# Optimization experiments

Measured on AMD Instinct MI355X. Metric: run time of the kernel, lower is better.

## Reference

```python
import jax, jax.numpy as jnp
import numpy as np

B, C, H, W, HEADS = 8, 96, 128, 128, 6  # dim=96, num_heads=6


def _conv(x, w, b=None, groups=1, pad=0):
    # NCHW conv, OIHW weights; groups for depthwise convs
    y = jax.lax.conv_general_dilated(
        x, w, window_strides=(1, 1), padding=[(pad, pad), (pad, pad)],
        dimension_numbers=('NCHW', 'OIHW', 'NCHW'), feature_group_count=groups)
    return y if b is None else y + b[None, :, None, None]


def setup_inputs() -> dict:
    key = jax.random.key(0)
    ks = jax.random.split(key, 12)
    s = lambda k, shape, fan: jax.random.normal(k, shape, jnp.float32) * (1.0 / np.sqrt(fan))
    return {
        "x": jax.random.normal(ks[0], (B, C, H, W), jnp.float32),
        "y": jax.random.normal(ks[1], (B, C, H, W), jnp.float32),
        "w_pos":   s(ks[2], (2 * C, 2 * C, 1, 1), 2 * C),      # pos 1x1, no bias
        "w_qv":    s(ks[3], (2 * C, C, 1, 1), C),              # qv_ 1x1
        "w_qv_dw": s(ks[4], (2 * C, 1, 3, 3), 9),              # qv depthwise 3x3
        "w_kv":    s(ks[5], (2 * C, C, 1, 1), C),              # kv 1x1
        "w_kv_dw": s(ks[6], (2 * C, 1, 3, 3), 9),              # kv depthwise 3x3
        "w_proj":  s(ks[7], (2 * C, C, 1, 1), C),              # project_out 1x1
        "w_fuse":  s(ks[8], (C, 2 * C, 3, 3), 2 * C * 9),      # v_fuse 3x3 (bias=True)
        "b_fuse":  jnp.zeros((C,), jnp.float32),
        "temperature": jnp.ones((HEADS, 1, 1), jnp.float32),
    }


def reference(x, y, w_pos, w_qv, w_qv_dw, w_kv, w_kv_dw, w_proj, w_fuse, b_fuse, temperature):
    b, c, h, w = x.shape
    xy_pos = _conv(jnp.concatenate([x, y], axis=1), w_pos)
    qv_ = _conv(_conv(x, w_qv), w_qv_dw, groups=2 * c, pad=1)
    kv = _conv(_conv(y, w_kv), w_kv_dw, groups=2 * c, pad=1)
    q, v_ = jnp.split(qv_, 2, axis=1)
    k, v0 = jnp.split(kv, 2, axis=1)
    v = _conv(jnp.concatenate([v0, v_], axis=1), w_fuse, b_fuse, pad=1)
    ch = c // HEADS
    resh = lambda t: t.reshape(b, HEADS, ch, h * w)  # b head c (h w)
    qh, kh, vh = resh(q), resh(k), resh(v)
    # F.normalize(dim=-1): L2 over spatial positions, eps=1e-12
    nrm = lambda t: t / jnp.maximum(jnp.linalg.norm(t, axis=-1, keepdims=True), 1e-12)
    qh, kh = nrm(qh), nrm(kh)
    attn = jax.nn.softmax(jnp.einsum('bhcn,bhdn->bhcd', qh, kh) * temperature, axis=-1)
    out = jnp.einsum('bhcd,bhdn->bhcn', attn, vh).reshape(b, c, h, w)
    return _conv(out, w_proj) + xy_pos
```

## Files before the change

### kernel.cpp

```cpp
#include <hip/hip_runtime.h>
#include <math.h>

#define NB 8
#define NSP 16384
#define NHEADS 6
#define BT ((long)NB * NSP)

typedef __attribute__((ext_vector_type(8))) short bf8_t;
typedef __attribute__((ext_vector_type(4))) float f4_t;
typedef unsigned short u16;

#define MFMA(A,B,C) __builtin_amdgcn_mfma_f32_16x16x32_bf16((A),(B),(C),0,0,0)

__device__ __forceinline__ u16 f2b(float f) {
  union { float f; unsigned u; } v; v.f = f;
  unsigned r = v.u + 0x7FFFu + ((v.u >> 16) & 1u);
  return (u16)(r >> 16);
}
__device__ __forceinline__ float b2f(u16 h) {
  union { unsigned u; float f; } v; v.u = ((unsigned)h) << 16; return v.f;
}


__global__ __launch_bounds__(256)
void pack_w_k(const float* __restrict__ wqv, const float* __restrict__ wkv,
              const float* __restrict__ wpos, const float* __restrict__ wfuse,
              u16* __restrict__ wqv_b, u16* __restrict__ wkv_b,
              u16* __restrict__ wpos_b, u16* __restrict__ wfA) {
  int i = blockIdx.x * 256 + threadIdx.x;
  if (i < 18432) { wqv_b[i] = f2b(wqv[i]); wkv_b[i] = f2b(wkv[i]); }
  if (i < 36864) wpos_b[i] = f2b(wpos[i]);
  if (i < 165888) {
    int kl = i & 31; int rest = i >> 5;
    int oc = rest % 96, kc = rest / 96;
    int c6 = kc / 9, tap = kc % 9;
    int icf = c6 * 32 + kl;
    wfA[i] = f2b(wfuse[(oc * 192 + icf) * 9 + tap]);
  }
}

__global__ __launch_bounds__(256)
void tcast_k(const float* __restrict__ x, const float* __restrict__ y,
             u16* __restrict__ xb, u16* __restrict__ yb) {
  const float* src = blockIdx.y ? y : x;
  u16* dst = blockIdx.y ? yb : xb;
  int t = threadIdx.x;
  long n  = (long)blockIdx.x * 64 + (t & 63);
  long b  = n >> 14; long ni = n & 16383;
  int c8b = t >> 6;
  for (int i = 0; i < 3; ++i) {
    int c8 = c8b + i * 4;
    bf8_t pk;
#pragma unroll
    for (int j = 0; j < 8; ++j)
      pk[j] = (short)f2b(src[(b * 96 + c8 * 8 + j) * NSP + ni]);
    *(bf8_t*)(dst + ((long)c8 * BT + n) * 8) = pk;
  }
}

__global__ __launch_bounds__(256)
void conv1x1_k(const u16* __restrict__ Bx, const u16* __restrict__ A,
               u16* __restrict__ out) {
  int t = threadIdx.x, w = t >> 6, lane = t & 63;
  int q = lane >> 4, l15 = lane & 15;
  long n0 = (long)blockIdx.x * 64;
  f4_t acc[3][4] = {};
#pragma unroll
  for (int kc = 0; kc < 3; ++kc) {
    bf8_t af[3], bfr[4];
#pragma unroll
    for (int mf = 0; mf < 3; ++mf)
      af[mf] = *(const bf8_t*)(A + (w * 48 + mf * 16 + l15) * 96 + kc * 32 + q * 8);
#pragma unroll
    for (int nf = 0; nf < 4; ++nf)
      bfr[nf] = *(const bf8_t*)(Bx + ((long)(kc * 4 + q) * BT + n0 + nf * 16 + l15) * 8);
#pragma unroll
    for (int mf = 0; mf < 3; ++mf)
#pragma unroll
      for (int nf = 0; nf < 4; ++nf)
        acc[mf][nf] = MFMA(af[mf], bfr[nf], acc[mf][nf]);
  }
#pragma unroll
  for (int mf = 0; mf < 3; ++mf)
#pragma unroll
    for (int nf = 0; nf < 4; ++nf) {
      union { u16 us[4]; uint2 v; } pk;
#pragma unroll
      for (int r = 0; r < 4; ++r) pk.us[r] = f2b(acc[mf][nf][r]);
      long n = n0 + nf * 16 + l15;
      int g = w * 6 + mf * 2 + (q >> 1);
      *(uint2*)(out + ((long)g * BT + n) * 8 + (q & 1) * 4) = pk.v;
    }
}

__global__ __launch_bounds__(256)
void dw_k(const u16* __restrict__ qv0, const u16* __restrict__ kv0,
          const float* __restrict__ wqvd, const float* __restrict__ wkvd,
          u16* __restrict__ qL, u16* __restrict__ kL, u16* __restrict__ fin) {
  int t = threadIdx.x;
  int sel = blockIdx.y;
  int bx = blockIdx.x;
  int gq = bx % 6;
  int rowid = bx / 6;
  long b = rowid >> 7; int r = rowid & 127;
  int wv = __builtin_amdgcn_readfirstlane(t >> 6);
  int g = gq * 4 + wv;
  int l = t & 63;
  int c0 = l * 2;

  const u16* src  = sel ? kv0 : qv0;
  const float* wd = sel ? wkvd : wqvd;

  float wgt[8][9];
#pragma unroll
  for (int cc = 0; cc < 8; ++cc)
#pragma unroll
    for (int tp = 0; tp < 9; ++tp)
      wgt[cc][tp] = wd[g * 72 + cc * 9 + tp];

  const u16* sg = src + (long)g * BT * 8;
  float acc[2][8] = {};
#pragma unroll
  for (int dy = -1; dy <= 1; ++dy) {
    int rr = r + dy;
    if ((unsigned)rr >= 128u) continue;
    long nb = (b << 14) + ((long)rr << 7);
    float xq[4][8];
#pragma unroll
    for (int j = 0; j < 4; ++j) {
      int col = c0 - 1 + j;
      uint4 cv = make_uint4(0u, 0u, 0u, 0u);
      if ((unsigned)col < 128u)
        cv = *(const uint4*)(sg + (nb + col) * 8);
      const unsigned* cu = (const unsigned*)&cv;
#pragma unroll
      for (int k = 0; k < 4; ++k) {
        union { unsigned u; float f; } lo, hi;
        lo.u = cu[k] << 16; hi.u = cu[k] & 0xFFFF0000u;
        xq[j][2 * k] = lo.f; xq[j][2 * k + 1] = hi.f;
      }
    }
#pragma unroll
    for (int dx = 0; dx < 3; ++dx) {
      int tp = (dy + 1) * 3 + dx;
#pragma unroll
      for (int px = 0; px < 2; ++px)
#pragma unroll
        for (int cc = 0; cc < 8; ++cc)
          acc[px][cc] += wgt[cc][tp] * xq[px + dx][cc];
    }
  }
  u16* dst; long gi;
  if (g < 12) { dst = sel ? kL : qL; gi = g; }
  else        { dst = fin; gi = sel ? (g - 12) : g; }
  u16* dp = dst + (gi * BT + (b << 14) + ((long)r << 7) + c0) * 8;
#pragma unroll
  for (int px = 0; px < 2; ++px) {
    union { u16 us[8]; uint4 v; } pk;
#pragma unroll
    for (int cc = 0; cc < 8; ++cc) pk.us[cc] = f2b(acc[px][cc]);
    *(uint4*)(dp + px * 8) = pk.v;
  }
}

__global__ __launch_bounds__(512)
void fuse_k(const u16* __restrict__ fin, const u16* __restrict__ wfA,
            const float* __restrict__ bfuse, u16* __restrict__ vout) {
  __shared__ __align__(16) u16 AL[2][192 * 36];
  int t = threadIdx.x, w = t >> 6, lane = t & 63;
  int q = lane >> 4, l15 = lane & 15;
  int bid = (int)blockIdx.x;
  bid = (bid & 7) * 64 + (bid >> 3);
  long n0 = (long)bid * 256;
  long b = n0 >> 14; int nimg0 = (int)(n0 & 16383);

  f4_t acc[6][2];
#pragma unroll
  for (int mf = 0; mf < 6; ++mf) {
#pragma unroll
    for (int rg = 0; rg < 4; ++rg) {
      float bv = bfuse[mf * 16 + q * 4 + rg];
      acc[mf][0][rg] = bv; acc[mf][1][rg] = bv;
    }
  }
  int ni_[2], r_[2], pw_[2];
#pragma unroll
  for (int nf = 0; nf < 2; ++nf) {
    ni_[nf] = nimg0 + w * 32 + nf * 16 + l15;
    r_[nf] = ni_[nf] >> 7; pw_[nf] = ni_[nf] & 127;
  }
  for (int i = t; i < 768; i += 512)
    *(f4_t*)(&AL[0][(i >> 2) * 36 + (i & 3) * 8]) = *(const f4_t*)(wfA + i * 8);
  __syncthreads();

  for (int kc2 = 0; kc2 < 27; ++kc2) {
    int cur = kc2 & 1;
    if (kc2 < 26) {
      const u16* srcw = wfA + (kc2 + 1) * 6144;
      for (int i = t; i < 768; i += 512)
        *(f4_t*)(&AL[cur ^ 1][(i >> 2) * 36 + (i & 3) * 8]) = *(const f4_t*)(srcw + i * 8);
    }
#pragma unroll
    for (int h = 0; h < 2; ++h) {
      int kc = kc2 * 2 + h;
      int c6 = kc / 9, tap = kc % 9;
      int dy = tap / 3 - 1, dx = tap % 3 - 1;
      const u16* src = fin + (long)(c6 * 4 + q) * BT * 8;
      bf8_t bfr[2];
#pragma unroll
      for (int nf = 0; nf < 2; ++nf) {
        bf8_t v = {0,0,0,0,0,0,0,0};
        int rr = r_[nf] + dy, cc = pw_[nf] + dx;
        if ((unsigned)rr < 128u && (unsigned)cc < 128u)
          v = *(const bf8_t*)(src + ((b << 14) + (long)ni_[nf] + dy * 128 + dx) * 8);
        bfr[nf] = v;
      }
      bf8_t af[6];
#pragma unroll
      for (int mf = 0; mf < 6; ++mf)
        af[mf] = *(const bf8_t*)(&AL[cur][(h * 96 + mf * 16 + l15) * 36 + q * 8]);
#pragma unroll
      for (int mf = 0; mf < 6; ++mf) {
        acc[mf][0] = MFMA(af[mf], bfr[0], acc[mf][0]);
        acc[mf][1] = MFMA(af[mf], bfr[1], acc[mf][1]);
      }
    }
    __syncthreads();
  }
#pragma unroll
  for (int mf = 0; mf < 6; ++mf)
#pragma unroll
    for (int nf = 0; nf < 2; ++nf) {
      union { u16 us[4]; uint2 v; } pk;
#pragma unroll
      for (int rg = 0; rg < 4; ++rg) pk.us[rg] = f2b(acc[mf][nf][rg]);
      long n = n0 + w * 32 + nf * 16 + l15;
      int gg = mf * 2 + (q >> 1);
      *(uint2*)(vout + ((long)gg * BT + n) * 8 + (q & 1) * 4) = pk.v;
    }
}

__global__ __launch_bounds__(256)
void ssq_k(const u16* __restrict__ qL, const u16* __restrict__ kL,
           float* __restrict__ ssq) {
  int c8 = blockIdx.x;
  int b = blockIdx.y >> 1, z = blockIdx.y & 1;
  const u16* src = (z ? kL : qL) + ((long)c8 * BT + (b << 14)) * 8;
  float ss[8] = {};
  int n0 = blockIdx.z * 4096, nend = n0 + 4096;
  for (int n = n0 + threadIdx.x; n < nend; n += 256) {
    bf8_t v = *(const bf8_t*)(src + (long)n * 8);
#pragma unroll
    for (int j = 0; j < 8; ++j) { float f = b2f((u16)v[j]); ss[j] += f * f; }
  }
#pragma unroll
  for (int off = 32; off; off >>= 1)
#pragma unroll
    for (int j = 0; j < 8; ++j) ss[j] += __shfl_down(ss[j], off);
  __shared__ float red[4][8];
  int lane = threadIdx.x & 63, wv = threadIdx.x >> 6;
  if (!lane)
#pragma unroll
    for (int j = 0; j < 8; ++j) red[wv][j] = ss[j];
  __syncthreads();
  if (threadIdx.x < 8) {
    int j = threadIdx.x;
    float tot = red[0][j] + red[1][j] + red[2][j] + red[3][j];
    atomicAdd(&ssq[(z * NB + b) * 96 + c8 * 8 + j], tot);
  }
}

__global__ __launch_bounds__(256)
void qk_k(const u16* __restrict__ qL, const u16* __restrict__ kL,
          float* __restrict__ logits) {
  int s = blockIdx.x, h = blockIdx.y, b = blockIdx.z;
  int t = threadIdx.x, c = t >> 4, d = t & 15;
  __shared__ u16 Qs[64 * 16], Ks[64 * 16];
  float acc = 0.f;
  int p = t >> 2, c4 = (t & 3) * 4;
  int ch2 = 2 * h + (c4 >> 3), e = c4 & 7;
  long cb = (long)ch2 * BT + (b << 14) + s * 512;
  for (int it = 0; it < 8; ++it) {
    __syncthreads();
    long a = (cb + it * 64 + p) * 8 + e;
    *(uint2*)(&Qs[p * 16 + c4]) = *(const uint2*)(qL + a);
    *(uint2*)(&Ks[p * 16 + c4]) = *(const uint2*)(kL + a);
    __syncthreads();
#pragma unroll 8
    for (int pp = 0; pp < 64; ++pp)
      acc += b2f(Qs[pp * 16 + c]) * b2f(Ks[pp * 16 + d]);
  }
  atomicAdd(&logits[((b * NHEADS + h) * 16 + c) * 16 + d], acc);
}

__global__ __launch_bounds__(256)
void softmax_k(const float* __restrict__ logits, const float* __restrict__ ssq,
               const float* __restrict__ temp, float* __restrict__ attn) {
  int t0 = blockIdx.x * 256 + threadIdx.x;
  if (t0 >= NB * 96) return;
  int b = t0 / 96, c96 = t0 % 96;
  int h = c96 >> 4, c = c96 & 15;
  float iq = 1.f / fmaxf(sqrtf(ssq[b * 96 + c96]), 1e-12f);
  float tp = temp[h];
  const float* lp = logits + ((b * NHEADS + h) * 16 + c) * 16;
  const float* sk = ssq + NB * 96 + b * 96 + h * 16;
  float s[16], mx = -3.4e38f;
#pragma unroll
  for (int d = 0; d < 16; ++d) {
    float ik = 1.f / fmaxf(sqrtf(sk[d]), 1e-12f);
    float l = lp[d] * iq * ik * tp;
    s[d] = l; mx = fmaxf(mx, l);
  }
  float sum = 0.f;
#pragma unroll
  for (int d = 0; d < 16; ++d) { s[d] = __expf(s[d] - mx); sum += s[d]; }
  float rr = 1.f / sum;
  float* ap = attn + ((b * NHEADS + h) * 16 + c) * 16;
#pragma unroll
  for (int d = 0; d < 16; ++d) ap[d] = s[d] * rr;
}

__global__ __launch_bounds__(256)
void wattn_k(const float* __restrict__ wproj, const float* __restrict__ attn,
             u16* __restrict__ Wp) {
  int b = blockIdx.x, t = threadIdx.x;
  __shared__ float at[1536];
  for (int i = t; i < 1536; i += 256) at[i] = attn[b * 1536 + i];
  __syncthreads();
  for (int i = t; i < 192 * 96; i += 256) {
    int oc = i / 96, e = i % 96;
    int h = e >> 4, d = e & 15;
    float s = 0.f;
#pragma unroll
    for (int c = 0; c < 16; ++c)
      s += wproj[oc * 96 + h * 16 + c] * at[(h * 16 + c) * 16 + d];
    Wp[(long)b * 18432 + i] = f2b(s);
  }
}

__global__ __launch_bounds__(256)
void final_k(const u16* __restrict__ Wp, const u16* __restrict__ wpos_b,
             const u16* __restrict__ v, const u16* __restrict__ xb,
             const u16* __restrict__ yb, float* __restrict__ out) {
  int t = threadIdx.x, w = t >> 6, lane = t & 63;
  int q = lane >> 4, l15 = lane & 15;
  long n0 = (long)blockIdx.x * 64;
  long b = n0 >> 14; int ni0 = (int)(n0 & 16383);
  f4_t acc[3][4] = {};
  const u16* Ab0 = Wp + b * 18432;
#pragma unroll
  for (int kc = 0; kc < 9; ++kc) {
    const u16 *Asrc, *Bsrc; int astr, koff, gB;
    if (kc < 3)      { Asrc = Ab0;    astr = 96;  koff = kc * 32;            Bsrc = v;  gB = kc * 4 + q; }
    else if (kc < 6) { Asrc = wpos_b; astr = 192; koff = (kc - 3) * 32;      Bsrc = xb; gB = (kc - 3) * 4 + q; }
    else             { Asrc = wpos_b; astr = 192; koff = 96 + (kc - 6) * 32; Bsrc = yb; gB = (kc - 6) * 4 + q; }
    bf8_t af[3], bfr[4];
#pragma unroll
    for (int mf = 0; mf < 3; ++mf)
      af[mf] = *(const bf8_t*)(Asrc + (w * 48 + mf * 16 + l15) * astr + koff + q * 8);
#pragma unroll
    for (int nf = 0; nf < 4; ++nf)
      bfr[nf] = *(const bf8_t*)(Bsrc + ((long)gB * BT + n0 + nf * 16 + l15) * 8);
#pragma unroll
    for (int mf = 0; mf < 3; ++mf)
#pragma unroll
      for (int nf = 0; nf < 4; ++nf)
        acc[mf][nf] = MFMA(af[mf], bfr[nf], acc[mf][nf]);
  }
#pragma unroll
  for (int mf = 0; mf < 3; ++mf)
#pragma unroll
    for (int nf = 0; nf < 4; ++nf)
#pragma unroll
      for (int rg = 0; rg < 4; ++rg) {
        int oc = w * 48 + mf * 16 + q * 4 + rg;
        out[(b * 192 + oc) * (long)NSP + ni0 + nf * 16 + l15] = acc[mf][nf][rg];
      }
}

extern "C" void kernel_launch(void* const* d_in, const int* in_sizes, int n_in,
                              void* d_out, int out_size, void* d_ws, size_t ws_size,
                              hipStream_t stream) {
  const float* x     = (const float*)d_in[0];
  const float* y     = (const float*)d_in[1];
  const float* wpos  = (const float*)d_in[2];
  const float* wqv   = (const float*)d_in[3];
  const float* wqvd  = (const float*)d_in[4];
  const float* wkv   = (const float*)d_in[5];
  const float* wkvd  = (const float*)d_in[6];
  const float* wproj = (const float*)d_in[7];
  const float* wfuse = (const float*)d_in[8];
  const float* bfuse = (const float*)d_in[9];
  const float* temp  = (const float*)d_in[10];
  float* out = (float*)d_out;
  char*  ws  = (char*)d_ws;

  u16*   xb     = (u16*)(ws);
  u16*   yb     = (u16*)(ws + 25165824);
  u16*   qL     = (u16*)(ws + 50331648);
  u16*   kL     = (u16*)(ws + 75497472);
  u16*   fin    = (u16*)(ws + 100663296);
  u16*   v      = (u16*)(ws + 150994944);
  u16*   wqv_b  = (u16*)(ws + 176160768);
  u16*   wkv_b  = (u16*)(ws + 176197632);
  u16*   wpos_b = (u16*)(ws + 176234496);
  u16*   wfA    = (u16*)(ws + 176308224);
  u16*   Wp     = (u16*)(ws + 176640000);
  float* ssq    = (float*)(ws + 176934912);
  float* logits = (float*)(ws + 176941056);
  float* attn   = (float*)(ws + 176990208);

  u16* qv0 = (u16*)d_out;
  u16* kv0 = (u16*)d_out + (size_t)24 * BT * 8;

  dim3 blk(256);
  pack_w_k<<<648, blk, 0, stream>>>(wqv, wkv, wpos, wfuse, wqv_b, wkv_b, wpos_b, wfA);
  tcast_k<<<dim3(2048, 2), blk, 0, stream>>>(x, y, xb, yb);
  conv1x1_k<<<2048, blk, 0, stream>>>(xb, wqv_b, qv0);
  conv1x1_k<<<2048, blk, 0, stream>>>(yb, wkv_b, kv0);
  dw_k<<<dim3(6144, 2), blk, 0, stream>>>(qv0, kv0, wqvd, wkvd, qL, kL, fin);
  hipMemsetAsync(ssq, 0, 6144 + 49152, stream);
  fuse_k<<<512, dim3(512), 0, stream>>>(fin, wfA, bfuse, v);
  ssq_k<<<dim3(12, 16, 4), blk, 0, stream>>>(qL, kL, ssq);
  qk_k<<<dim3(32, NHEADS, NB), blk, 0, stream>>>(qL, kL, logits);
  softmax_k<<<3, blk, 0, stream>>>(logits, ssq, temp, attn);
  wattn_k<<<NB, blk, 0, stream>>>(wproj, attn, Wp);
  final_k<<<2048, blk, 0, stream>>>(Wp, wpos_b, v, xb, yb, out);
}
```

Measured before the change: 478.8 us.

## Fuse sum-of-squares into depthwise conv and process four rows per thread

The depthwise 3x3 kernel now computes four output rows per thread with a sliding six-row input window, so input rows are reused across outputs instead of reloaded. It also accumulates the per-channel sum of squares of the bf16-rounded q/k outputs and atomically adds them into ssq, which removes the separate ssq_k pass that re-read qL and kL. In exchange, register pressure rises from the larger accumulator, the grid shrinks to a quarter of the blocks, and there are more atomics per launch.

```diff
diff --git a/kernel.cpp b/kernel.cpp
--- a/kernel.cpp
+++ b/kernel.cpp
@@ -96,13 +96,15 @@
 __global__ __launch_bounds__(256)
 void dw_k(const u16* __restrict__ qv0, const u16* __restrict__ kv0,
           const float* __restrict__ wqvd, const float* __restrict__ wkvd,
-          u16* __restrict__ qL, u16* __restrict__ kL, u16* __restrict__ fin) {
+          u16* __restrict__ qL, u16* __restrict__ kL, u16* __restrict__ fin,
+          float* __restrict__ ssq) {
   int t = threadIdx.x;
   int sel = blockIdx.y;
   int bx = blockIdx.x;
   int gq = bx % 6;
   int rowid = bx / 6;
-  long b = rowid >> 7; int r = rowid & 127;
+  long b = rowid >> 5; int rg = rowid & 31;
+  int r0 = rg * 4;
   int wv = __builtin_amdgcn_readfirstlane(t >> 6);
   int g = gq * 4 + wv;
   int l = t & 63;
@@ -119,47 +121,75 @@
       wgt[cc][tp] = wd[g * 72 + cc * 9 + tp];
 
   const u16* sg = src + (long)g * BT * 8;
-  float acc[2][8] = {};
-#pragma unroll
-  for (int dy = -1; dy <= 1; ++dy) {
-    int rr = r + dy;
-    if ((unsigned)rr >= 128u) continue;
-    long nb = (b << 14) + ((long)rr << 7);
-    float xq[4][8];
-#pragma unroll
-    for (int j = 0; j < 4; ++j) {
-      int col = c0 - 1 + j;
-      uint4 cv = make_uint4(0u, 0u, 0u, 0u);
-      if ((unsigned)col < 128u)
-        cv = *(const uint4*)(sg + (nb + col) * 8);
-      const unsigned* cu = (const unsigned*)&cv;
-#pragma unroll
-      for (int k = 0; k < 4; ++k) {
-        union { unsigned u; float f; } lo, hi;
-        lo.u = cu[k] << 16; hi.u = cu[k] & 0xFFFF0000u;
-        xq[j][2 * k] = lo.f; xq[j][2 * k + 1] = hi.f;
-      }
-    }
-#pragma unroll
-    for (int dx = 0; dx < 3; ++dx) {
-      int tp = (dy + 1) * 3 + dx;
-#pragma unroll
-      for (int px = 0; px < 2; ++px)
-#pragma unroll
-        for (int cc = 0; cc < 8; ++cc)
-          acc[px][cc] += wgt[cc][tp] * xq[px + dx][cc];
-    }
-  }
   u16* dst; long gi;
   if (g < 12) { dst = sel ? kL : qL; gi = g; }
   else        { dst = fin; gi = sel ? (g - 12) : g; }
-  u16* dp = dst + (gi * BT + (b << 14) + ((long)r << 7) + c0) * 8;
-#pragma unroll
-  for (int px = 0; px < 2; ++px) {
-    union { u16 us[8]; uint4 v; } pk;
-#pragma unroll
-    for (int cc = 0; cc < 8; ++cc) pk.us[cc] = f2b(acc[px][cc]);
-    *(uint4*)(dp + px * 8) = pk.v;
+  u16* dpb = dst + (gi * BT + (b << 14)) * 8;
+
+  float acc[4][2][8] = {};
+  float ssl[8] = {};
+#pragma unroll
+  for (int j = 0; j < 6; ++j) {
+    int rr = r0 - 1 + j;
+    if ((unsigned)rr < 128u) {
+      long nb = (b << 14) + ((long)rr << 7);
+      float xq[4][8];
+#pragma unroll
+      for (int jj = 0; jj < 4; ++jj) {
+        int col = c0 - 1 + jj;
+        uint4 cv = make_uint4(0u, 0u, 0u, 0u);
+        if ((unsigned)col < 128u)
+          cv = *(const uint4*)(sg + (nb + col) * 8);
+        const unsigned* cu = (const unsigned*)&cv;
+#pragma unroll
+        for (int k = 0; k < 4; ++k) {
+          union { unsigned u; float f; } lo, hi;
+          lo.u = cu[k] << 16; hi.u = cu[k] & 0xFFFF0000u;
+          xq[jj][2 * k] = lo.f; xq[jj][2 * k + 1] = hi.f;
+        }
+      }
+#pragma unroll
+      for (int i = 0; i < 4; ++i) {
+        if (i > j || i + 2 < j) continue;
+        int tr = j - i;
+#pragma unroll
+        for (int dx = 0; dx < 3; ++dx) {
+          int tp = tr * 3 + dx;
+#pragma unroll
+          for (int px = 0; px < 2; ++px)
+#pragma unroll
+            for (int cc = 0; cc < 8; ++cc)
+              acc[i][px][cc] += wgt[cc][tp] * xq[px + dx][cc];
+        }
+      }
+    }
+    if (j >= 2) {
+      int i = j - 2;
+      u16* dp = dpb + ((((long)(r0 + i)) << 7) + c0) * 8;
+#pragma unroll
+      for (int px = 0; px < 2; ++px) {
+        union { u16 us[8]; uint4 v; } pk;
+#pragma unroll
+        for (int cc = 0; cc < 8; ++cc) pk.us[cc] = f2b(acc[i][px][cc]);
+        *(uint4*)(dp + px * 8) = pk.v;
+        if (g < 12) {
+#pragma unroll
+          for (int cc = 0; cc < 8; ++cc) {
+            float f = b2f(pk.us[cc]); ssl[cc] += f * f;
+          }
+        }
+      }
+    }
+  }
+  if (g < 12) {
+#pragma unroll
+    for (int off = 32; off; off >>= 1)
+#pragma unroll
+      for (int cc = 0; cc < 8; ++cc) ssl[cc] += __shfl_down(ssl[cc], off);
+    if (l == 0)
+#pragma unroll
+      for (int cc = 0; cc < 8; ++cc)
+        atomicAdd(&ssq[(sel * NB + (int)b) * 96 + g * 8 + cc], ssl[cc]);
   }
 }
 
@@ -238,36 +268,6 @@
       int gg = mf * 2 + (q >> 1);
       *(uint2*)(vout + ((long)gg * BT + n) * 8 + (q & 1) * 4) = pk.v;
     }
-}
-
-__global__ __launch_bounds__(256)
-void ssq_k(const u16* __restrict__ qL, const u16* __restrict__ kL,
-           float* __restrict__ ssq) {
-  int c8 = blockIdx.x;
-  int b = blockIdx.y >> 1, z = blockIdx.y & 1;
-  const u16* src = (z ? kL : qL) + ((long)c8 * BT + (b << 14)) * 8;
-  float ss[8] = {};
-  int n0 = blockIdx.z * 4096, nend = n0 + 4096;
-  for (int n = n0 + threadIdx.x; n < nend; n += 256) {
-    bf8_t v = *(const bf8_t*)(src + (long)n * 8);
-#pragma unroll
-    for (int j = 0; j < 8; ++j) { float f = b2f((u16)v[j]); ss[j] += f * f; }
-  }
-#pragma unroll
-  for (int off = 32; off; off >>= 1)
-#pragma unroll
-    for (int j = 0; j < 8; ++j) ss[j] += __shfl_down(ss[j], off);
-  __shared__ float red[4][8];
-  int lane = threadIdx.x & 63, wv = threadIdx.x >> 6;
-  if (!lane)
-#pragma unroll
-    for (int j = 0; j < 8; ++j) red[wv][j] = ss[j];
-  __syncthreads();
-  if (threadIdx.x < 8) {
-    int j = threadIdx.x;
-    float tot = red[0][j] + red[1][j] + red[2][j] + red[3][j];
-    atomicAdd(&ssq[(z * NB + b) * 96 + c8 * 8 + j], tot);
-  }
 }
 
 __global__ __launch_bounds__(256)
@@ -418,10 +418,9 @@
   tcast_k<<<dim3(2048, 2), blk, 0, stream>>>(x, y, xb, yb);
   conv1x1_k<<<2048, blk, 0, stream>>>(xb, wqv_b, qv0);
   conv1x1_k<<<2048, blk, 0, stream>>>(yb, wkv_b, kv0);
-  dw_k<<<dim3(6144, 2), blk, 0, stream>>>(qv0, kv0, wqvd, wkvd, qL, kL, fin);
   hipMemsetAsync(ssq, 0, 6144 + 49152, stream);
+  dw_k<<<dim3(1536, 2), blk, 0, stream>>>(qv0, kv0, wqvd, wkvd, qL, kL, fin, ssq);
   fuse_k<<<512, dim3(512), 0, stream>>>(fin, wfA, bfuse, v);
-  ssq_k<<<dim3(12, 16, 4), blk, 0, stream>>>(qL, kL, ssq);
   qk_k<<<dim3(32, NHEADS, NB), blk, 0, stream>>>(qL, kL, logits);
   softmax_k<<<3, blk, 0, stream>>>(logits, ssq, temp, attn);
   wattn_k<<<NB, blk, 0, stream>>>(wproj, attn, Wp);
```

Result: faster. 469.2 us (-2.0%).
